# Performance work log

Measured on AMD Instinct MI355X. Metric: run time of the kernel, lower is better.

## Reference

```python
import jax, jax.numpy as jnp
import numpy as np
import math

B, S, D_MODEL, N_HEAD, D_HEAD, D_FFN = 1, 2048, 1024, 16, 64, 4096
EPS = 1e-6


def setup_inputs() -> dict:
    key = jax.random.key(0)
    ks = jax.random.split(key, 10)
    scale = 0.02
    x = jax.random.normal(ks[0], (B, S, D_MODEL), dtype=jnp.float32)
    # RoPE frequencies: freqs_cis[s, i] = exp(1j * s * theta_i), theta_i = 10000^{-2i/d_head}
    half = D_HEAD // 2
    inv_freq = 1.0 / (10000.0 ** (jnp.arange(0, half, dtype=jnp.float32) * 2.0 / D_HEAD))
    angles = jnp.arange(S, dtype=jnp.float32)[:, None] * inv_freq[None, :]  # [S, half]
    freqs_cos = jnp.cos(angles)
    freqs_sin = jnp.sin(angles)
    wq = jax.random.normal(ks[1], (D_MODEL, N_HEAD * D_HEAD), dtype=jnp.float32) * scale
    wk = jax.random.normal(ks[2], (D_MODEL, N_HEAD * D_HEAD), dtype=jnp.float32) * scale
    wv = jax.random.normal(ks[3], (D_MODEL, N_HEAD * D_HEAD), dtype=jnp.float32) * scale
    wo = jax.random.normal(ks[4], (N_HEAD * D_HEAD, D_MODEL), dtype=jnp.float32) * scale
    w1 = jax.random.normal(ks[5], (D_MODEL, D_FFN), dtype=jnp.float32) * scale
    w2 = jax.random.normal(ks[6], (D_FFN, D_MODEL), dtype=jnp.float32) * scale
    w3 = jax.random.normal(ks[7], (D_MODEL, D_FFN), dtype=jnp.float32) * scale
    attn_norm_w = jnp.ones((D_MODEL,), dtype=jnp.float32)
    ffn_norm_w = jnp.ones((D_MODEL,), dtype=jnp.float32)
    return {"x": x, "freqs_cos": freqs_cos, "freqs_sin": freqs_sin,
            "wq": wq, "wk": wk, "wv": wv, "wo": wo,
            "w1": w1, "w2": w2, "w3": w3,
            "attn_norm_w": attn_norm_w, "ffn_norm_w": ffn_norm_w}


def _rmsnorm(x, w):
    xf = x.astype(jnp.float32)
    inv = jax.lax.rsqrt(jnp.mean(xf * xf, axis=-1, keepdims=True) + EPS)
    return (xf * inv).astype(x.dtype) * w


def _rope(t, cos, sin):
    # t: [B, S, H, D]; treat last dim as interleaved (even, odd) complex pairs
    b, s, h, d = t.shape
    tr = t.astype(jnp.float32).reshape(b, s, h, d // 2, 2)
    te, to = tr[..., 0], tr[..., 1]
    c = cos[None, :, None, :]
    sn = sin[None, :, None, :]
    out = jnp.stack([te * c - to * sn, te * sn + to * c], axis=-1)
    return out.reshape(b, s, h, d).astype(t.dtype)


def reference(x, freqs_cos, freqs_sin, wq, wk, wv, wo, w1, w2, w3, attn_norm_w, ffn_norm_w):
    bsz, seqlen, _ = x.shape
    # --- attention sub-block ---
    hin = _rmsnorm(x, attn_norm_w)
    q = (hin @ wq).reshape(bsz, seqlen, N_HEAD, D_HEAD)
    k = (hin @ wk).reshape(bsz, seqlen, N_HEAD, D_HEAD)
    v = (hin @ wv).reshape(bsz, seqlen, N_HEAD, D_HEAD)
    q = _rope(q, freqs_cos, freqs_sin)
    k = _rope(k, freqs_cos, freqs_sin)
    # [B, H, S, S] scores, softmax in fp32 (no causal mask in original)
    scores = jnp.einsum('bqhd,bkhd->bhqk', q, k) / math.sqrt(D_HEAD)
    probs = jax.nn.softmax(scores.astype(jnp.float32), axis=-1).astype(q.dtype)
    attn = jnp.einsum('bhqk,bkhd->bqhd', probs, v).reshape(bsz, seqlen, N_HEAD * D_HEAD)
    h = x + attn @ wo
    # --- SwiGLU FFN sub-block ---
    f = _rmsnorm(h, ffn_norm_w)
    ffn = (jax.nn.silu(f @ w1) * (f @ w3)) @ w2
    return h + ffn
```

## Files before the change

### kernel.cpp

```cpp
#include <hip/hip_runtime.h>
#include <stdint.h>
#include <stddef.h>

using bf16x8 = __attribute__((ext_vector_type(8))) __bf16;
using f32x4  = __attribute__((ext_vector_type(4))) float;
using f32x16 = __attribute__((ext_vector_type(16))) float;

__device__ __forceinline__ float bf2f(unsigned short u) {
  union { unsigned int i; float f; } v; v.i = ((unsigned int)u) << 16; return v.f;
}
__device__ __forceinline__ unsigned short f2bf(float f) {
  union { float f; unsigned int i; } v; v.f = f;
  unsigned int r = v.i + 0x7fffu + ((v.i >> 16) & 1u);
  return (unsigned short)(r >> 16);
}
__device__ __forceinline__ unsigned short f2bf_trunc(float f) {
  union { float f; unsigned int i; } v; v.f = f;
  return (unsigned short)(v.i >> 16);
}
__device__ __forceinline__ unsigned int pk_trunc(float a, float b) {
  union { float f; unsigned int i; } x, y; x.f = a; y.f = b;
  return (x.i >> 16) | (y.i & 0xffff0000u);
}
__device__ __forceinline__ bf16x8 mk_bf16x8(unsigned int a, unsigned int b,
                                            unsigned int c, unsigned int d) {
  union { unsigned int u[4]; bf16x8 v; } x;
  x.u[0] = a; x.u[1] = b; x.u[2] = c; x.u[3] = d; return x.v;
}
__device__ __forceinline__ void async16(const void* g, void* l) {
  __builtin_amdgcn_global_load_lds(
      (const __attribute__((address_space(1))) unsigned int*)g,
      (__attribute__((address_space(3))) unsigned int*)l, 16, 0, 0);
}

#define S_LEN 2048
#define DMODEL 1024
#define NHEAD 16
#define DHEAD 64
#define DFFN 4096

struct T4 {
  const float *s0, *s1, *s2, *s3;
  unsigned short *d0, *d1, *d2, *d3;
};
__global__ __launch_bounds__(256) void transpose4_k(T4 j) {
  const float* in = blockIdx.z == 0 ? j.s0 : blockIdx.z == 1 ? j.s1 : blockIdx.z == 2 ? j.s2 : j.s3;
  unsigned short* out = blockIdx.z == 0 ? j.d0 : blockIdx.z == 1 ? j.d1 : blockIdx.z == 2 ? j.d2 : j.d3;
  __shared__ unsigned short tile[32][33];
  const int tx = threadIdx.x & 31;
  const int ty = threadIdx.x >> 5;
  const int bc = blockIdx.x * 32;
  const int br = blockIdx.y * 32;
#pragma unroll
  for (int i = 0; i < 4; ++i)
    tile[ty + i * 8][tx] = f2bf(in[(size_t)(br + ty + i * 8) * 1024 + bc + tx]);
  __syncthreads();
#pragma unroll
  for (int i = 0; i < 4; ++i)
    out[(size_t)(bc + ty + i * 8) * 1024 + br + tx] = tile[tx][ty + i * 8];
}

__global__ __launch_bounds__(256) void transpose13_k(
    const float* __restrict__ w1, const float* __restrict__ w3,
    unsigned short* __restrict__ out) {
  const float* in = blockIdx.z ? w3 : w1;
  const int rb = blockIdx.z * 32;
  __shared__ unsigned short tile[32][33];
  const int tx = threadIdx.x & 31;
  const int ty = threadIdx.x >> 5;
  const int bc = blockIdx.x * 32;
  const int br = blockIdx.y * 32;
#pragma unroll
  for (int i = 0; i < 4; ++i)
    tile[ty + i * 8][tx] = f2bf(in[(size_t)(br + ty + i * 8) * 4096 + bc + tx]);
  __syncthreads();
#pragma unroll
  for (int i = 0; i < 4; ++i) {
    int c = bc + ty + i * 8;
    int dest = (c >> 5) * 64 + rb + (c & 31);
    out[(size_t)dest * 1024 + br + tx] = tile[tx][ty + i * 8];
  }
}

__global__ __launch_bounds__(256) void transpose_w2_k(
    const float* __restrict__ in, unsigned short* __restrict__ out) {
  __shared__ unsigned short tile[32][33];
  const int tx = threadIdx.x & 31;
  const int ty = threadIdx.x >> 5;
  const int bc = blockIdx.x * 32;
  const int br = blockIdx.y * 32;
#pragma unroll
  for (int i = 0; i < 4; ++i)
    tile[ty + i * 8][tx] = f2bf(in[(size_t)(br + ty + i * 8) * 1024 + bc + tx]);
  __syncthreads();
#pragma unroll
  for (int i = 0; i < 4; ++i)
    out[(size_t)(bc + ty + i * 8) * 4096 + br + tx] = tile[tx][ty + i * 8];
}

__global__ __launch_bounds__(256) void vtrans_k(
    const unsigned short* __restrict__ QKV, unsigned short* __restrict__ VtG) {
  __shared__ unsigned short tile[32][33];
  const int tx = threadIdx.x & 31;
  const int ty = threadIdx.x >> 5;
  const int bc = blockIdx.x * 32;
  const int br = blockIdx.y * 32;
#pragma unroll
  for (int i = 0; i < 4; ++i)
    tile[ty + i * 8][tx] = QKV[(size_t)(br + ty + i * 8) * 3072 + 2048 + bc + tx];
  __syncthreads();
#pragma unroll
  for (int i = 0; i < 4; ++i)
    VtG[(size_t)(bc + ty + i * 8) * 2048 + br + tx] = tile[tx][ty + i * 8];
}

__global__ __launch_bounds__(256) void rmsnorm_k(
    const float* __restrict__ X, const float* __restrict__ W,
    unsigned short* __restrict__ Y) {
  const int row = blockIdx.x;
  const int t = threadIdx.x;
  const int lane = t & 63, w = t >> 6;
  const float* x = X + (size_t)row * DMODEL;
  float xs[4];
  float s = 0.f;
#pragma unroll
  for (int i = 0; i < 4; ++i) {
    xs[i] = x[t * 4 + i];
    s += xs[i] * xs[i];
  }
#pragma unroll
  for (int m = 1; m < 64; m <<= 1) s += __shfl_xor(s, m, 64);
  __shared__ float red[4];
  if (lane == 0) red[w] = s;
  __syncthreads();
  float tot = red[0] + red[1] + red[2] + red[3];
  float inv = rsqrtf(tot * (1.0f / DMODEL) + 1e-6f);
#pragma unroll
  for (int i = 0; i < 4; ++i)
    Y[(size_t)row * DMODEL + t * 4 + i] = f2bf(xs[i] * inv * W[t * 4 + i]);
}

template <int MODE>
__global__ __launch_bounds__(256) void gemm_bt(
    const unsigned short* __restrict__ A, int lda,
    const unsigned short* __restrict__ BT,
    void* __restrict__ Cout,
    int K, int N) {
  __shared__ unsigned short As[128 * 64];
  __shared__ unsigned short Bs[128 * 64];
  const int t = threadIdx.x;
  const int lane = t & 63;
  const int w = t >> 6;
  const int qr = (w >> 1) * 64, qc = (w & 1) * 64;
  const int l31 = lane & 31, half = lane >> 5;
  const int m0 = blockIdx.y * 128, n0 = blockIdx.x * 128;

  f32x16 acc[2][2] = {};

  int srow[4], scol[4];
#pragma unroll
  for (int p = 0; p < 4; ++p) {
    int off = p * 2048 + t * 8;
    int r = off >> 6;
    srow[p] = r;
    scol[p] = (((off >> 3) & 7) ^ (r & 7)) * 8;
  }

  for (int k0 = 0; k0 < K; k0 += 64) {
    __syncthreads();
#pragma unroll
    for (int p = 0; p < 4; ++p) {
      int off = p * 2048 + t * 8;
      async16(A + (size_t)(m0 + srow[p]) * lda + (k0 + scol[p]), &As[off]);
      async16(BT + (size_t)(n0 + srow[p]) * K + (k0 + scol[p]), &Bs[off]);
    }
    __syncthreads();
#pragma unroll
    for (int ks = 0; ks < 4; ++ks) {
      const int ch = ((ks * 2 + half) ^ (l31 & 7)) * 8;
      bf16x8 a0 = *(const bf16x8*)&As[(qr + l31) * 64 + ch];
      bf16x8 a1 = *(const bf16x8*)&As[(qr + 32 + l31) * 64 + ch];
      bf16x8 b0 = *(const bf16x8*)&Bs[(qc + l31) * 64 + ch];
      bf16x8 b1 = *(const bf16x8*)&Bs[(qc + 32 + l31) * 64 + ch];
      acc[0][0] = __builtin_amdgcn_mfma_f32_32x32x16_bf16(a0, b0, acc[0][0], 0, 0, 0);
      acc[0][1] = __builtin_amdgcn_mfma_f32_32x32x16_bf16(a0, b1, acc[0][1], 0, 0, 0);
      acc[1][0] = __builtin_amdgcn_mfma_f32_32x32x16_bf16(a1, b0, acc[1][0], 0, 0, 0);
      acc[1][1] = __builtin_amdgcn_mfma_f32_32x32x16_bf16(a1, b1, acc[1][1], 0, 0, 0);
    }
  }

  {
    unsigned short* C = (unsigned short*)Cout;
#pragma unroll
    for (int rt = 0; rt < 2; ++rt)
#pragma unroll
      for (int ct = 0; ct < 2; ++ct)
#pragma unroll
        for (int reg = 0; reg < 16; ++reg) {
          int rr = m0 + qr + rt * 32 + (reg & 3) + 8 * (reg >> 2) + 4 * half;
          int cc = n0 + qc + ct * 32 + l31;
          C[(size_t)rr * N + cc] = f2bf(acc[rt][ct][reg]);
        }
  }
}

__device__ __forceinline__ void mfma8(f32x16& c0, f32x16& c1,
                                      const bf16x8 (&a)[2][4],
                                      const bf16x8 (&b)[4]) {
  __builtin_amdgcn_s_setprio(1);
#pragma unroll
  for (int ks = 0; ks < 4; ++ks) {
    c0 = __builtin_amdgcn_mfma_f32_32x32x16_bf16(a[0][ks], b[ks], c0, 0, 0, 0);
    c1 = __builtin_amdgcn_mfma_f32_32x32x16_bf16(a[1][ks], b[ks], c1, 0, 0, 0);
  }
  __builtin_amdgcn_s_setprio(0);
}

__global__ __launch_bounds__(512, 2) void gemm256_silu(
    const unsigned short* __restrict__ A,
    const unsigned short* __restrict__ BT,
    unsigned short* __restrict__ F) {
  __shared__ unsigned short lds[65536];
  const int t = threadIdx.x;
  const int l = t & 63, l31 = l & 31, half = l >> 5;
  const int w = t >> 6;
  const int wm = w >> 2, wn = w & 3;

  const int orig = blockIdx.x;
  const int bx = (orig & 7) * 4 + ((orig >> 3) & 3);
  const int by = orig >> 5;
  const int m0 = by * 256, n0 = bx * 256;

  const int rA = t >> 3;
  const int sc = ((t & 7) ^ ((t >> 3) & 7)) * 8;
  const int lo = t * 8;

#define STAGE_A(h, tile, d)                                                    \
  { async16(A + (size_t)(m0 + (h) * 128 + rA) * 1024 + (tile) * 64 + sc,       \
            &lds[(d) * 32768 + (h) * 8192 + lo]);                              \
    async16(A + (size_t)(m0 + (h) * 128 + 64 + rA) * 1024 + (tile) * 64 + sc,  \
            &lds[(d) * 32768 + (h) * 8192 + 4096 + lo]); }
#define STAGE_B(h, tile, d)                                                    \
  { async16(BT + (size_t)(n0 + (h) * 128 + rA) * 1024 + (tile) * 64 + sc,      \
            &lds[(d) * 32768 + 16384 + (h) * 8192 + lo]);                      \
    async16(BT + (size_t)(n0 + (h) * 128 + 64 + rA) * 1024 + (tile) * 64 + sc, \
            &lds[(d) * 32768 + 16384 + (h) * 8192 + 4096 + lo]); }

  const int arow = wm * 128 + l31;
  const int brow = wn * 64 + l31;
  int kc[4];
#pragma unroll
  for (int ks = 0; ks < 4; ++ks) kc[ks] = ((ks * 2 + half) ^ (l31 & 7)) * 8;

#define LDA(d, mt, ks) (*(const bf16x8*)&lds[(d) * 32768 + (arow + (mt) * 32) * 64 + kc[ks]])
#define LDB(d, nt, ks) (*(const bf16x8*)&lds[(d) * 32768 + 16384 + (brow + (nt) * 32) * 64 + kc[ks]])

  f32x16 acc[4][2] = {};
  bf16x8 afr[2][4], bfr[2][4];

  STAGE_A(0, 0, 0); STAGE_A(1, 0, 0); STAGE_B(0, 0, 0); STAGE_B(1, 0, 0);
  STAGE_A(0, 1, 1); STAGE_A(1, 1, 1);
  asm volatile("s_waitcnt vmcnt(4)" ::: "memory");
  __builtin_amdgcn_s_barrier();

#pragma unroll 1
  for (int i = 0; i < 8; ++i) {
    const int t1 = 2 * i + 1, t2 = 2 * i + 2, t3 = 2 * i + 3;
    const bool more = i < 7;

#pragma unroll
    for (int ks = 0; ks < 4; ++ks) {
      afr[0][ks] = LDA(0, 0, ks);
      afr[1][ks] = LDA(0, 1, ks);
      bfr[0][ks] = LDB(0, 0, ks);
    }
    STAGE_B(0, t1, 1);
    __builtin_amdgcn_s_barrier();
    mfma8(acc[0][0], acc[1][0], afr, bfr[0]);
    __builtin_amdgcn_s_barrier();

#pragma unroll
    for (int ks = 0; ks < 4; ++ks) bfr[1][ks] = LDB(0, 1, ks);
    STAGE_B(1, t1, 1);
    __builtin_amdgcn_s_barrier();
    mfma8(acc[0][1], acc[1][1], afr, bfr[1]);
    __builtin_amdgcn_s_barrier();

#pragma unroll
    for (int ks = 0; ks < 4; ++ks) {
      afr[0][ks] = LDA(0, 2, ks);
      afr[1][ks] = LDA(0, 3, ks);
    }
    if (more) STAGE_B(0, t2, 0);
    __builtin_amdgcn_s_barrier();
    mfma8(acc[2][1], acc[3][1], afr, bfr[1]);
    __builtin_amdgcn_s_barrier();

    if (more) {
      STAGE_B(1, t2, 0);
      STAGE_A(0, t2, 0);
      asm volatile("s_waitcnt vmcnt(8)" ::: "memory");
    } else {
      asm volatile("s_waitcnt vmcnt(2)" ::: "memory");
    }
    __builtin_amdgcn_s_barrier();
    mfma8(acc[2][0], acc[3][0], afr, bfr[0]);
    __builtin_amdgcn_s_barrier();

#pragma unroll
    for (int ks = 0; ks < 4; ++ks) {
      afr[0][ks] = LDA(1, 0, ks);
      afr[1][ks] = LDA(1, 1, ks);
      bfr[0][ks] = LDB(1, 0, ks);
    }
    if (more) {
      STAGE_A(1, t2, 0);
      asm volatile("s_waitcnt vmcnt(8)" ::: "memory");
    } else {
      asm volatile("s_waitcnt vmcnt(0)" ::: "memory");
    }
    __builtin_amdgcn_s_barrier();
    mfma8(acc[0][0], acc[1][0], afr, bfr[0]);
    __builtin_amdgcn_s_barrier();

#pragma unroll
    for (int ks = 0; ks < 4; ++ks) bfr[1][ks] = LDB(1, 1, ks);
    __builtin_amdgcn_s_barrier();
    mfma8(acc[0][1], acc[1][1], afr, bfr[1]);
    __builtin_amdgcn_s_barrier();

#pragma unroll
    for (int ks = 0; ks < 4; ++ks) {
      afr[0][ks] = LDA(1, 2, ks);
      afr[1][ks] = LDA(1, 3, ks);
    }
    __builtin_amdgcn_s_barrier();
    mfma8(acc[2][1], acc[3][1], afr, bfr[1]);
    __builtin_amdgcn_s_barrier();

    if (more) {
      STAGE_A(0, t3, 1);
      STAGE_A(1, t3, 1);
      asm volatile("s_waitcnt vmcnt(4)" ::: "memory");
    } else {
      asm volatile("s_waitcnt vmcnt(0)" ::: "memory");
    }
    __builtin_amdgcn_s_barrier();
    mfma8(acc[2][0], acc[3][0], afr, bfr[0]);
    __builtin_amdgcn_s_barrier();
  }

#undef STAGE_A
#undef STAGE_B
#undef LDA
#undef LDB

  const int ccol = (n0 >> 1) + wn * 32 + l31;
  const int rbase = m0 + wm * 128 + 4 * half;
#pragma unroll
  for (int mt = 0; mt < 4; ++mt)
#pragma unroll
    for (int reg = 0; reg < 16; ++reg) {
      int rr = rbase + mt * 32 + (reg & 3) + 8 * (reg >> 2);
      float a1v = acc[mt][0][reg];
      float a3v = acc[mt][1][reg];
      float f = a1v / (1.f + __expf(-a1v)) * a3v;
      F[(size_t)rr * 4096 + ccol] = f2bf(f);
    }
}

struct PtrPair { float* p0; float* p1; };

__global__ __launch_bounds__(256) void gemm_bt_sk(
    const unsigned short* __restrict__ A, int lda,
    const unsigned short* __restrict__ BT,
    PtrPair parts, int Kc, int Ktot, int N) {
  __shared__ unsigned short As[64 * 64];
  __shared__ unsigned short Bs[128 * 64];
  const int t = threadIdx.x;
  const int lane = t & 63;
  const int w = t >> 6;
  const int qr = (w >> 1) * 32, qc = (w & 1) * 64;
  const int l31 = lane & 31, half = lane >> 5;
  const int m0 = blockIdx.y * 64, n0 = blockIdx.x * 128;
  const int kb = blockIdx.z * Kc;

  f32x16 acc[2] = {};

  for (int k0 = 0; k0 < Kc; k0 += 64) {
    __syncthreads();
#pragma unroll
    for (int p = 0; p < 2; ++p) {
      int off = p * 2048 + t * 8;
      int r = off >> 6;
      int sc = (((off >> 3) & 7) ^ (r & 7)) * 8;
      async16(A + (size_t)(m0 + r) * lda + (kb + k0 + sc), &As[off]);
    }
#pragma unroll
    for (int p = 0; p < 4; ++p) {
      int off = p * 2048 + t * 8;
      int r = off >> 6;
      int sc = (((off >> 3) & 7) ^ (r & 7)) * 8;
      async16(BT + (size_t)(n0 + r) * Ktot + (kb + k0 + sc), &Bs[off]);
    }
    __syncthreads();
#pragma unroll
    for (int ks = 0; ks < 4; ++ks) {
      const int ch = ((ks * 2 + half) ^ (l31 & 7)) * 8;
      bf16x8 a0 = *(const bf16x8*)&As[(qr + l31) * 64 + ch];
      bf16x8 b0 = *(const bf16x8*)&Bs[(qc + l31) * 64 + ch];
      bf16x8 b1 = *(const bf16x8*)&Bs[(qc + 32 + l31) * 64 + ch];
      acc[0] = __builtin_amdgcn_mfma_f32_32x32x16_bf16(a0, b0, acc[0], 0, 0, 0);
      acc[1] = __builtin_amdgcn_mfma_f32_32x32x16_bf16(a0, b1, acc[1], 0, 0, 0);
    }
  }

  float* C = blockIdx.z ? parts.p1 : parts.p0;
#pragma unroll
  for (int ct = 0; ct < 2; ++ct)
#pragma unroll
    for (int reg = 0; reg < 16; ++reg) {
      int rr = m0 + qr + (reg & 3) + 8 * (reg >> 2) + 4 * half;
      int cc = n0 + qc + ct * 32 + l31;
      C[(size_t)rr * N + cc] = acc[ct][reg];
    }
}

__global__ __launch_bounds__(256) void reduce2_k(
    const float4* __restrict__ P0, const float4* __restrict__ P1,
    const float4* __restrict__ R, float4* __restrict__ Out, int nvec) {
  int i = blockIdx.x * 256 + threadIdx.x;
  if (i >= nvec) return;
  float4 a = P0[i], b = P1[i], r = R[i];
  float4 o;
  o.x = a.x + b.x + r.x;
  o.y = a.y + b.y + r.y;
  o.z = a.z + b.z + r.z;
  o.w = a.w + b.w + r.w;
  Out[i] = o;
}

__global__ __launch_bounds__(256) void rope_k(
    unsigned short* __restrict__ QKV,
    const float* __restrict__ cosp,
    const float* __restrict__ sinp) {
  int idx = blockIdx.x * 256 + threadIdx.x;
  int s = idx >> 9;
  int rem = idx & 511;
  int h = rem >> 5;
  int i = rem & 31;
  float c = cosp[s * 32 + i];
  float sn = sinp[s * 32 + i];
  size_t off = (size_t)s * 3072 + h * 64 + 2 * i;
  {
    float e = bf2f(QKV[off]), o = bf2f(QKV[off + 1]);
    QKV[off] = f2bf(e * c - o * sn);
    QKV[off + 1] = f2bf(e * sn + o * c);
  }
  {
    float e = bf2f(QKV[off + 1024]), o = bf2f(QKV[off + 1025]);
    QKV[off + 1024] = f2bf((e * c - o * sn) * 0.125f);
    QKV[off + 1025] = f2bf((e * sn + o * c) * 0.125f);
  }
}

__global__ __launch_bounds__(256) void attn_k(
    const unsigned short* __restrict__ QKV,
    const unsigned short* __restrict__ VtG,
    float* __restrict__ O0, float* __restrict__ O1,
    float* __restrict__ L) {
  const int h = blockIdx.y;
  const int qb = blockIdx.x;
  const int z = blockIdx.z;
  const int t = threadIdx.x;
  const int lane = t & 63;
  const int l31 = lane & 31, half = lane >> 5;
  const int w = t >> 6;
  const int q0 = qb * 128 + w * 32;
  const int kbase = z * 1024;

  __shared__ unsigned short Kt[2][64 * 64];
  __shared__ unsigned short Vt[2][64 * 64];

  const unsigned short* Kp = QKV + 1024 + h * 64;
  const unsigned short* Vg = VtG + (size_t)h * 64 * 2048;

  bf16x8 qf[4];
#pragma unroll
  for (int ks = 0; ks < 4; ++ks)
    qf[ks] = *(const bf16x8*)(QKV + (size_t)(q0 + l31) * 3072 + h * 64 + ks * 16 + half * 8);

#pragma unroll
  for (int p = 0; p < 2; ++p) {
    int off = p * 2048 + t * 8;
    int r = off >> 6;
    int sc8 = (((off >> 3) & 7) ^ (r & 7)) * 8;
    async16(Kp + (size_t)(kbase + r) * 3072 + sc8, &Kt[0][off]);
    async16(Vg + (size_t)r * 2048 + kbase + sc8, &Vt[0][off]);
  }
  asm volatile("s_waitcnt vmcnt(0)" ::: "memory");
  __syncthreads();

  f32x16 oacc[2] = {};
  float l_r = 0.f;

#pragma unroll 1
  for (int kt = 0; kt < 16; ++kt) {
    const int cur = kt & 1;
    if (kt + 1 < 16) {
      int kb2 = kbase + (kt + 1) * 64;
#pragma unroll
      for (int p = 0; p < 2; ++p) {
        int off = p * 2048 + t * 8;
        int r = off >> 6;
        int sc8 = (((off >> 3) & 7) ^ (r & 7)) * 8;
        async16(Kp + (size_t)(kb2 + r) * 3072 + sc8, &Kt[cur ^ 1][off]);
        async16(Vg + (size_t)r * 2048 + kb2 + sc8, &Vt[cur ^ 1][off]);
      }
    }

    f32x16 st[2] = {};
#pragma unroll
    for (int ks = 0; ks < 4; ++ks) {
      const int ch = ((2 * ks + half) ^ (l31 & 7)) * 8;
      bf16x8 k0 = *(const bf16x8*)&Kt[cur][l31 * 64 + ch];
      bf16x8 k1 = *(const bf16x8*)&Kt[cur][(32 + l31) * 64 + ch];
      st[0] = __builtin_amdgcn_mfma_f32_32x32x16_bf16(k0, qf[ks], st[0], 0, 0, 0);
      st[1] = __builtin_amdgcn_mfma_f32_32x32x16_bf16(k1, qf[ks], st[1], 0, 0, 0);
    }

    float psum = 0.f;
#pragma unroll
    for (int b = 0; b < 2; ++b)
#pragma unroll
      for (int r = 0; r < 16; ++r) {
        float e = __expf(st[b][r]);
        st[b][r] = e;
        psum += e;
      }
    l_r += psum;

    unsigned int pklo[8], pkhi[8];
#pragma unroll
    for (int b = 0; b < 2; ++b)
#pragma unroll
      for (int m = 0; m < 4; ++m) {
        pklo[b * 4 + m] = pk_trunc(st[b][4 * m + 0], st[b][4 * m + 1]);
        pkhi[b * 4 + m] = pk_trunc(st[b][4 * m + 2], st[b][4 * m + 3]);
      }

#pragma unroll
    for (int ks = 0; ks < 4; ++ks) {
      unsigned int keep_lo = half ? pklo[2 * ks + 1] : pklo[2 * ks];
      unsigned int keep_hi = half ? pkhi[2 * ks + 1] : pkhi[2 * ks];
      unsigned int pass_lo = half ? pklo[2 * ks] : pklo[2 * ks + 1];
      unsigned int pass_hi = half ? pkhi[2 * ks] : pkhi[2 * ks + 1];
      unsigned int olo = (unsigned int)__shfl_xor((int)pass_lo, 32, 64);
      unsigned int ohi = (unsigned int)__shfl_xor((int)pass_hi, 32, 64);
      unsigned int w0 = half ? olo : keep_lo;
      unsigned int w1 = half ? ohi : keep_hi;
      unsigned int w2 = half ? keep_lo : olo;
      unsigned int w3 = half ? keep_hi : ohi;
      bf16x8 af = mk_bf16x8(w0, w1, w2, w3);
      const int ch = ((2 * ks + half) ^ (l31 & 7)) * 8;
      bf16x8 v0 = *(const bf16x8*)&Vt[cur][l31 * 64 + ch];
      bf16x8 v1 = *(const bf16x8*)&Vt[cur][(32 + l31) * 64 + ch];
      oacc[0] = __builtin_amdgcn_mfma_f32_32x32x16_bf16(af, v0, oacc[0], 0, 0, 0);
      oacc[1] = __builtin_amdgcn_mfma_f32_32x32x16_bf16(af, v1, oacc[1], 0, 0, 0);
    }

    __syncthreads();
  }

  float lt = l_r + __shfl_xor(l_r, 32, 64);
  float* Op = z ? O1 : O0;
#pragma unroll
  for (int db = 0; db < 2; ++db)
#pragma unroll
    for (int reg = 0; reg < 16; ++reg) {
      int q = (reg & 3) + 8 * (reg >> 2) + 4 * half;
      Op[(size_t)(q0 + q) * DMODEL + h * 64 + db * 32 + l31] = oacc[db][reg];
    }
  if (half == 0)
    L[(size_t)(h * 2 + z) * S_LEN + q0 + l31] = lt;
}

__global__ __launch_bounds__(256) void attn_combine_k(
    const float4* __restrict__ O0, const float4* __restrict__ O1,
    const float* __restrict__ L, unsigned short* __restrict__ Attn) {
  int i = blockIdx.x * 256 + threadIdx.x;
  int e0 = i * 4;
  int s = e0 >> 10;
  int c = e0 & 1023;
  int h = c >> 6;
  float la = L[(size_t)(h * 2) * S_LEN + s];
  float lb = L[(size_t)(h * 2 + 1) * S_LEN + s];
  float inv = 1.f / (la + lb);
  float4 a = O0[i], b = O1[i];
  ushort4 r;
  r.x = f2bf((a.x + b.x) * inv);
  r.y = f2bf((a.y + b.y) * inv);
  r.z = f2bf((a.z + b.z) * inv);
  r.w = f2bf((a.w + b.w) * inv);
  *(ushort4*)(Attn + e0) = r;
}

extern "C" void kernel_launch(void* const* d_in, const int* in_sizes, int n_in,
                              void* d_out, int out_size, void* d_ws, size_t ws_size,
                              hipStream_t stream) {
  (void)in_sizes; (void)n_in; (void)out_size; (void)ws_size;
  const float* x    = (const float*)d_in[0];
  const float* fcos = (const float*)d_in[1];
  const float* fsin = (const float*)d_in[2];
  const float* wq   = (const float*)d_in[3];
  const float* wk   = (const float*)d_in[4];
  const float* wv   = (const float*)d_in[5];
  const float* wo   = (const float*)d_in[6];
  const float* w1   = (const float*)d_in[7];
  const float* w2   = (const float*)d_in[8];
  const float* w3   = (const float*)d_in[9];
  const float* anw  = (const float*)d_in[10];
  const float* fnw  = (const float*)d_in[11];
  float* out = (float*)d_out;
  char* ws = (char*)d_ws;

  unsigned short* WqkvT = (unsigned short*)(ws + 0);
  unsigned short* VtG   = (unsigned short*)(ws + 0);
  float*          Lbuf  = (float*)(ws + 4194304);
  unsigned short* WoT   = (unsigned short*)(ws + 6291456);
  unsigned short* QKV   = (unsigned short*)(ws + 8388608);
  unsigned short* Attn  = (unsigned short*)(ws + 20971520);
  float* Oa             = (float*)(ws + 25165824);
  float* Ob             = (float*)(ws + 37748736);
  float* P0a            = (float*)(ws + 8388608);
  float* P1a            = (float*)(ws + 25165824);
  unsigned short* F     = (unsigned short*)(ws + 0);
  float* P0b            = (float*)(ws + 16777216);
  float* P1b            = (float*)(ws + 25165824);
  unsigned short* Hin   = (unsigned short*)(ws + 33554432);
  float*          Hres  = (float*)        (ws + 37748736);
  unsigned short* W13I  = (unsigned short*)(ws + 46137344);
  unsigned short* W2T   = (unsigned short*)(ws + 62914560);

  transpose4_k<<<dim3(32, 32, 4), 256, 0, stream>>>(
      T4{wq, wk, wv, wo, WqkvT, WqkvT + 1048576, WqkvT + 2097152, WoT});
  transpose13_k<<<dim3(128, 32, 2), 256, 0, stream>>>(w1, w3, W13I);
  transpose_w2_k<<<dim3(32, 128), 256, 0, stream>>>(w2, W2T);

  rmsnorm_k<<<2048, 256, 0, stream>>>(x, anw, Hin);
  gemm_bt<0><<<dim3(24, 16), 256, 0, stream>>>(Hin, 1024, WqkvT, QKV, 1024, 3072);
  rope_k<<<4096, 256, 0, stream>>>(QKV, fcos, fsin);
  vtrans_k<<<dim3(32, 64), 256, 0, stream>>>(QKV, VtG);
  attn_k<<<dim3(16, 16, 2), 256, 0, stream>>>(QKV, VtG, Oa, Ob, Lbuf);
  attn_combine_k<<<2048, 256, 0, stream>>>((const float4*)Oa, (const float4*)Ob, Lbuf, Attn);
  gemm_bt_sk<<<dim3(8, 32, 2), 256, 0, stream>>>(Attn, 1024, WoT, PtrPair{P0a, P1a}, 512, 1024, 1024);
  reduce2_k<<<2048, 256, 0, stream>>>((const float4*)P0a, (const float4*)P1a,
                                      (const float4*)x, (float4*)Hres, 524288);

  rmsnorm_k<<<2048, 256, 0, stream>>>(Hres, fnw, Hin);
  gemm256_silu<<<dim3(256), 512, 0, stream>>>(Hin, W13I, F);
  gemm_bt_sk<<<dim3(8, 32, 2), 256, 0, stream>>>(F, 4096, W2T, PtrPair{P0b, P1b}, 2048, 4096, 1024);
  reduce2_k<<<2048, 256, 0, stream>>>((const float4*)P0b, (const float4*)P1b,
                                      (const float4*)Hres, (float4*)out, 524288);
}
```

Baseline: 299.1 us.

## Reorder async staging schedule and strengthen LDS swizzle in SiLU GEMM

Reworks the double-buffered prefetch schedule in the 256x256 SwiGLU GEMM so that A and B half-tiles are issued in a different order, spreading one async load across each MFMA phase with adjusted vmcnt waits. It also reorders the MFMA sub-blocks. A second change adds an extra XOR term to the LDS swizzle on both the store and load sides to reduce bank conflicts. The aim is smoother overlap of global loads with MFMA work and fewer LDS conflicts. It risks races or wrong results if the new wait counts do not match the outstanding loads.

```diff
diff --git a/kernel.cpp b/kernel.cpp
--- a/kernel.cpp
+++ b/kernel.cpp
@@ -232,7 +232,7 @@
   const int m0 = by * 256, n0 = bx * 256;
 
   const int rA = t >> 3;
-  const int sc = ((t & 7) ^ ((t >> 3) & 7)) * 8;
+  const int sc = ((t & 7) ^ ((t >> 3) & 7) ^ ((t >> 6) & 3)) * 8;
   const int lo = t * 8;
 
 #define STAGE_A(h, tile, d)                                                    \
@@ -248,9 +248,10 @@
 
   const int arow = wm * 128 + l31;
   const int brow = wn * 64 + l31;
+  const int gsw = (l31 & 7) ^ ((l31 >> 3) & 3);
   int kc[4];
 #pragma unroll
-  for (int ks = 0; ks < 4; ++ks) kc[ks] = ((ks * 2 + half) ^ (l31 & 7)) * 8;
+  for (int ks = 0; ks < 4; ++ks) kc[ks] = ((ks * 2 + half) ^ gsw) * 8;
 
 #define LDA(d, mt, ks) (*(const bf16x8*)&lds[(d) * 32768 + (arow + (mt) * 32) * 64 + kc[ks]])
 #define LDB(d, nt, ks) (*(const bf16x8*)&lds[(d) * 32768 + 16384 + (brow + (nt) * 32) * 64 + kc[ks]])
@@ -258,14 +259,16 @@
   f32x16 acc[4][2] = {};
   bf16x8 afr[2][4], bfr[2][4];
 
-  STAGE_A(0, 0, 0); STAGE_A(1, 0, 0); STAGE_B(0, 0, 0); STAGE_B(1, 0, 0);
-  STAGE_A(0, 1, 1); STAGE_A(1, 1, 1);
-  asm volatile("s_waitcnt vmcnt(4)" ::: "memory");
+  STAGE_B(0, 0, 0); STAGE_B(1, 0, 0); STAGE_A(0, 0, 0); STAGE_A(1, 0, 0);
+  STAGE_B(0, 1, 1); STAGE_B(1, 1, 1); STAGE_A(0, 1, 1);
+  asm volatile("s_waitcnt vmcnt(6)" ::: "memory");
   __builtin_amdgcn_s_barrier();
 
 #pragma unroll 1
   for (int i = 0; i < 8; ++i) {
-    const int t1 = 2 * i + 1, t2 = 2 * i + 2, t3 = 2 * i + 3;
+    const int b1t = 2 * i + 1;
+    const int a2 = 2 * i + 2;
+    const int b2 = 2 * i + 3;
     const bool more = i < 7;
 
 #pragma unroll
@@ -274,14 +277,14 @@
       afr[1][ks] = LDA(0, 1, ks);
       bfr[0][ks] = LDB(0, 0, ks);
     }
-    STAGE_B(0, t1, 1);
+    STAGE_A(1, b1t, 1);
     __builtin_amdgcn_s_barrier();
     mfma8(acc[0][0], acc[1][0], afr, bfr[0]);
     __builtin_amdgcn_s_barrier();
 
 #pragma unroll
     for (int ks = 0; ks < 4; ++ks) bfr[1][ks] = LDB(0, 1, ks);
-    STAGE_B(1, t1, 1);
+    if (more) STAGE_B(0, a2, 0);
     __builtin_amdgcn_s_barrier();
     mfma8(acc[0][1], acc[1][1], afr, bfr[1]);
     __builtin_amdgcn_s_barrier();
@@ -291,20 +294,19 @@
       afr[0][ks] = LDA(0, 2, ks);
       afr[1][ks] = LDA(0, 3, ks);
     }
-    if (more) STAGE_B(0, t2, 0);
+    if (more) STAGE_B(1, a2, 0);
+    __builtin_amdgcn_s_barrier();
+    mfma8(acc[2][0], acc[3][0], afr, bfr[0]);
+    __builtin_amdgcn_s_barrier();
+
+    if (more) {
+      STAGE_A(0, a2, 0);
+      asm volatile("s_waitcnt vmcnt(6)" ::: "memory");
+    } else {
+      asm volatile("s_waitcnt vmcnt(0)" ::: "memory");
+    }
     __builtin_amdgcn_s_barrier();
     mfma8(acc[2][1], acc[3][1], afr, bfr[1]);
-    __builtin_amdgcn_s_barrier();
-
-    if (more) {
-      STAGE_B(1, t2, 0);
-      STAGE_A(0, t2, 0);
-      asm volatile("s_waitcnt vmcnt(8)" ::: "memory");
-    } else {
-      asm volatile("s_waitcnt vmcnt(2)" ::: "memory");
-    }
-    __builtin_amdgcn_s_barrier();
-    mfma8(acc[2][0], acc[3][0], afr, bfr[0]);
     __builtin_amdgcn_s_barrier();
 
 #pragma unroll
@@ -313,40 +315,36 @@
       afr[1][ks] = LDA(1, 1, ks);
       bfr[0][ks] = LDB(1, 0, ks);
     }
+    if (more) STAGE_A(1, a2, 0);
+    __builtin_amdgcn_s_barrier();
+    mfma8(acc[0][0], acc[1][0], afr, bfr[0]);
+    __builtin_amdgcn_s_barrier();
+
+#pragma unroll
+    for (int ks = 0; ks < 4; ++ks) bfr[1][ks] = LDB(1, 1, ks);
+    if (more) STAGE_B(0, b2, 1);
+    __builtin_amdgcn_s_barrier();
+    mfma8(acc[0][1], acc[1][1], afr, bfr[1]);
+    __builtin_amdgcn_s_barrier();
+
+#pragma unroll
+    for (int ks = 0; ks < 4; ++ks) {
+      afr[0][ks] = LDA(1, 2, ks);
+      afr[1][ks] = LDA(1, 3, ks);
+    }
+    if (more) STAGE_B(1, b2, 1);
+    __builtin_amdgcn_s_barrier();
+    mfma8(acc[2][0], acc[3][0], afr, bfr[0]);
+    __builtin_amdgcn_s_barrier();
+
     if (more) {
-      STAGE_A(1, t2, 0);
-      asm volatile("s_waitcnt vmcnt(8)" ::: "memory");
+      STAGE_A(0, b2, 1);
+      asm volatile("s_waitcnt vmcnt(6)" ::: "memory");
     } else {
       asm volatile("s_waitcnt vmcnt(0)" ::: "memory");
     }
     __builtin_amdgcn_s_barrier();
-    mfma8(acc[0][0], acc[1][0], afr, bfr[0]);
-    __builtin_amdgcn_s_barrier();
-
-#pragma unroll
-    for (int ks = 0; ks < 4; ++ks) bfr[1][ks] = LDB(1, 1, ks);
-    __builtin_amdgcn_s_barrier();
-    mfma8(acc[0][1], acc[1][1], afr, bfr[1]);
-    __builtin_amdgcn_s_barrier();
-
-#pragma unroll
-    for (int ks = 0; ks < 4; ++ks) {
-      afr[0][ks] = LDA(1, 2, ks);
-      afr[1][ks] = LDA(1, 3, ks);
-    }
-    __builtin_amdgcn_s_barrier();
     mfma8(acc[2][1], acc[3][1], afr, bfr[1]);
-    __builtin_amdgcn_s_barrier();
-
-    if (more) {
-      STAGE_A(0, t3, 1);
-      STAGE_A(1, t3, 1);
-      asm volatile("s_waitcnt vmcnt(4)" ::: "memory");
-    } else {
-      asm volatile("s_waitcnt vmcnt(0)" ::: "memory");
-    }
-    __builtin_amdgcn_s_barrier();
-    mfma8(acc[2][0], acc[3][0], afr, bfr[0]);
     __builtin_amdgcn_s_barrier();
   }
 
```

After: 302.2 us. Within noise of the previous version (+1.0%).
